# Performance work log

Measured on AMD Instinct MI355X. Metric: run time of the kernel, lower is better.

The kernel has to match this reference:

```python
import jax, jax.numpy as jnp
import numpy as np

B, D, O = 1024, 512, 256


def setup_inputs() -> dict:
    key = jax.random.key(0)
    kx, kw, kt = jax.random.split(key, 3)
    x = jax.random.uniform(kx, (B, D), dtype=jnp.float32)
    w = jax.random.uniform(kw, (D, O), dtype=jnp.float32)
    t = jax.random.uniform(kt, (B, O), dtype=jnp.float32)
    return {"x": x, "w": w, "t": t}


def reference(x, w, t):
    xe = x[:, :, None]   # [B, D, 1]
    te = t[:, None, :]   # [B, 1, O]
    we = w[None, :, :]   # [1, D, O]

    x_comp = 1.0 - xe    # [B, D, 1]
    t_comp = 1.0 - te    # [B, 1, O]
    w_comp = 1.0 - we    # [1, D, O]

    # rel_x: [1, D, O]; sum over batch dim 0 of broadcasted min
    rel_x = 1.0 - (jnp.sum(jnp.minimum(x_comp, t_comp), axis=0, keepdims=True)
                   / jnp.sum(x_comp, axis=0, keepdims=True))
    # rel_w: [B, 1, O]; sum over D dim of broadcasted min
    rel_w = 1.0 - (jnp.sum(jnp.minimum(w_comp, t_comp), axis=-2, keepdims=True)
                   / jnp.sum(w_comp, axis=-2, keepdims=True))

    ind_x = jnp.argmin(jnp.maximum(xe, rel_x), axis=-2, keepdims=True)  # [B, 1, O]
    ind_w = jnp.argmin(jnp.maximum(rel_w, we), axis=-2, keepdims=True)  # [B, 1, O]

    inner_x = jnp.maximum(xe, jax.lax.stop_gradient(we))  # [B, D, O]
    inner_w = jnp.maximum(jax.lax.stop_gradient(xe), we)  # [B, D, O]

    chosen_x = jnp.take_along_axis(inner_x, ind_x, axis=-2).squeeze(-2)  # [B, O]
    chosen_w = jnp.take_along_axis(inner_w, ind_w, axis=-2).squeeze(-2)  # [B, O]
    return chosen_x, chosen_w
```

## Files before the change

kernel.cpp:

```cpp
#include <hip/hip_runtime.h>

#define BB 1024
#define DD 512
#define OO 256

__global__ __launch_bounds__(256) void kA(const float* __restrict__ x,
                                          const float* __restrict__ w,
                                          const float* __restrict__ t,
                                          float* __restrict__ xT,
                                          float* __restrict__ tT,
                                          float* __restrict__ wT,
                                          double* __restrict__ Sxp,
                                          double* __restrict__ part) {
  __shared__ float smem[8 * 136];
  int bid = blockIdx.x, tid = threadIdx.x;
  if (bid < 512) {
    float (*xl)[136] = (float(*)[136])smem;
    int dg = bid >> 3, sy = bid & 7;
    int d0 = dg * 8, b0 = sy * 128, o = tid;
    {
      int bb = tid >> 1, half = tid & 1;
      float4 g = *(const float4*)&x[(b0 + bb) * DD + d0 + half * 4];
      xl[half * 4 + 0][bb] = g.x;
      xl[half * 4 + 1][bb] = g.y;
      xl[half * 4 + 2][bb] = g.z;
      xl[half * 4 + 3][bb] = g.w;
    }
    __syncthreads();
    double acc[8] = {0, 0, 0, 0, 0, 0, 0, 0};
    for (int bb = 0; bb < 128; bb += 4) {
      float tv0 = t[(b0 + bb + 0) * OO + o];
      float tv1 = t[(b0 + bb + 1) * OO + o];
      float tv2 = t[(b0 + bb + 2) * OO + o];
      float tv3 = t[(b0 + bb + 3) * OO + o];
#pragma unroll
      for (int dd = 0; dd < 8; ++dd) {
        float4 xv = *(const float4*)&xl[dd][bb];
        double s01 = (double)fmaxf(xv.x, tv0) + (double)fmaxf(xv.y, tv1);
        double s23 = (double)fmaxf(xv.z, tv2) + (double)fmaxf(xv.w, tv3);
        acc[dd] += s01 + s23;
      }
    }
#pragma unroll
    for (int dd = 0; dd < 8; ++dd)
      part[(sy * DD + d0 + dd) * OO + o] = acc[dd];
  } else if (bid < 1024) {
    float (*tile)[33] = (float(*)[33])smem;
    int r = bid - 512;
    int b0 = (r & 31) * 32, d0 = (r >> 5) * 32;
    int tx = tid & 31, ty = tid >> 5;
    for (int i = 0; i < 32; i += 8)
      tile[ty + i][tx] = x[(b0 + ty + i) * DD + d0 + tx];
    __syncthreads();
    for (int i = 0; i < 32; i += 8)
      xT[(d0 + ty + i) * BB + b0 + tx] = tile[tx][ty + i];
  } else if (bid < 1280) {
    float (*tile)[33] = (float(*)[33])smem;
    int r = bid - 1024;
    int b0 = (r & 31) * 32, o0 = (r >> 5) * 32;
    int tx = tid & 31, ty = tid >> 5;
    for (int i = 0; i < 32; i += 8)
      tile[ty + i][tx] = t[(b0 + ty + i) * OO + o0 + tx];
    __syncthreads();
    for (int i = 0; i < 32; i += 8)
      tT[(o0 + ty + i) * BB + b0 + tx] = tile[tx][ty + i];
  } else if (bid < 1408) {
    float (*tile)[33] = (float(*)[33])smem;
    int r = bid - 1280;
    int d0 = (r & 15) * 32, o0 = (r >> 4) * 32;
    int tx = tid & 31, ty = tid >> 5;
    for (int i = 0; i < 32; i += 8)
      tile[ty + i][tx] = w[(d0 + ty + i) * OO + o0 + tx];
    __syncthreads();
    for (int i = 0; i < 32; i += 8)
      wT[(o0 + ty + i) * DD + d0 + tx] = tile[tx][ty + i];
  } else {
    int r = bid - 1408;
    int sy = r & 7, dh = r >> 3;
    int d = dh * 256 + tid, b0 = sy * 128;
    double s = 0.0;
    for (int b = b0; b < b0 + 128; ++b) s += 1.0 - (double)x[b * DD + d];
    Sxp[sy * DD + d] = s;
  }
}

__global__ __launch_bounds__(256) void kB(const float* __restrict__ wT,
                                          const double* __restrict__ Sxp,
                                          const double* __restrict__ part,
                                          float* __restrict__ sv_g,
                                          int* __restrict__ si_g,
                                          int* __restrict__ off_g,
                                          double* __restrict__ P_g,
                                          int* __restrict__ Mx_g,
                                          double* __restrict__ rv_g,
                                          int* __restrict__ ri_g,
                                          float* __restrict__ eb_g,
                                          double* __restrict__ hdrW,
                                          int* __restrict__ gmin_g) {
  int bid = blockIdx.x, tid = threadIdx.x;
  int lane = tid & 63, wid = tid >> 6;
  if (bid < OO) {
    int o = bid;
    __shared__ float sv[512];
    __shared__ int si[512];
    __shared__ int cnt[512];
    __shared__ int off[513];
    __shared__ double P[513];
    __shared__ int Mx[513];
    __shared__ double wsc[4];
    __shared__ int wmn[4];
    __shared__ unsigned long long wk[4];
    int i0 = 2 * tid, i1 = 2 * tid + 1;
    float w0 = wT[o * DD + i0], w1 = wT[o * DD + i1];
    cnt[i0] = 0; cnt[i1] = 0;
    __syncthreads();
    int q0 = min(511, max(0, (int)(w0 * 512.0f)));
    int q1 = min(511, max(0, (int)(w1 * 512.0f)));
    int sl0 = atomicAdd(&cnt[q0], 1);
    int sl1 = atomicAdd(&cnt[q1], 1);
    __syncthreads();
    {
      int e0 = cnt[i0], e1 = cnt[i1];
      int s = e0 + e1, v = s;
      for (int d = 1; d < 64; d <<= 1) {
        int u = __shfl_up(v, d);
        if (lane >= d) v += u;
      }
      if (lane == 63) wmn[wid] = v;
      __syncthreads();
      int wp = 0;
      for (int u = 0; u < wid; ++u) wp += wmn[u];
      int ex = wp + (v - s);
      off[i0] = ex; off[i1] = ex + e0;
      if (tid == 255) off[512] = ex + s;
      __syncthreads();
    }
    sv[off[q0] + sl0] = w0; si[off[q0] + sl0] = i0;
    sv[off[q1] + sl1] = w1; si[off[q1] + sl1] = i1;
    __syncthreads();
    for (int q = tid; q < 512; q += 256) {
      int s = off[q], e = off[q + 1];
      for (int i = s + 1; i < e; ++i) {
        int ki = si[i]; float kv = sv[i]; int j = i - 1;
        while (j >= s && si[j] > ki) { si[j + 1] = si[j]; sv[j + 1] = sv[j]; --j; }
        si[j + 1] = ki; sv[j + 1] = kv;
      }
    }
    __syncthreads();
    {
      double e0 = (double)sv[i0], e1 = (double)sv[i1];
      int m0 = si[i0], m1 = si[i1];
      double s = e0 + e1; int mm = min(m0, m1);
      double vs = s; int vm = mm;
      for (int d = 1; d < 64; d <<= 1) {
        double us = __shfl_up(vs, d);
        int um = __shfl_up(vm, d);
        if (lane >= d) { vs += us; vm = min(vm, um); }
      }
      double exs = __shfl_up(vs, 1);
      int exm = __shfl_up(vm, 1);
      if (lane == 0) { exs = 0.0; exm = 0x7fffffff; }
      if (lane == 63) { wsc[wid] = vs; wmn[wid] = vm; }
      __syncthreads();
      double wp = 0.0; int wm = 0x7fffffff;
      for (int u = 0; u < wid; ++u) { wp += wsc[u]; wm = min(wm, wmn[u]); }
      double EX = wp + exs; int EXM = min(wm, exm);
      P[i0] = EX; P[i1] = EX + e0;
      Mx[i0] = EXM; Mx[i1] = min(EXM, m0);
      if (tid == 255) { P[512] = EX + s; Mx[512] = min(EXM, mm); }
      __syncthreads();
    }
    {
      unsigned long long k0 = ((unsigned long long)__float_as_uint(sv[i0]) << 32) | (unsigned)si[i0];
      unsigned long long k1 = ((unsigned long long)__float_as_uint(sv[i1]) << 32) | (unsigned)si[i1];
      unsigned long long kk = k0 < k1 ? k0 : k1;
      for (int d = 32; d > 0; d >>= 1) {
        unsigned long long u = __shfl_down(kk, d);
        kk = u < kk ? u : kk;
      }
      if (lane == 0) wk[wid] = kk;
      __syncthreads();
      if (tid == 0) {
        unsigned long long g = wk[0];
        for (int u = 1; u < 4; ++u) g = wk[u] < g ? wk[u] : g;
        gmin_g[o] = (int)(g & 0xffffffffull);
      }
    }
    for (int i = tid; i < 512; i += 256) {
      sv_g[o * 512 + i] = sv[i];
      si_g[o * 512 + i] = si[i];
    }
    for (int i = tid; i < 513; i += 256) {
      off_g[o * 513 + i] = off[i];
      P_g[o * 513 + i] = P[i];
      Mx_g[o * 513 + i] = Mx[i];
    }
    if (tid == 0) { hdrW[o * 2 + 0] = 512.0 - P[512]; hdrW[o * 2 + 1] = P[512]; }
  } else {
    int o = bid - OO;
    __shared__ double rl[512];
    __shared__ int cnt2[512];
    __shared__ int roff[513];
    __shared__ double rv[512];
    __shared__ int ri[512];
    __shared__ float eb[512];
    __shared__ double wred[8];
    __shared__ int wint[4];
    int i0 = 2 * tid, i1 = 2 * tid + 1;
    {
      double sx0 = 0.0, sx1 = 0.0, a0 = 0.0, a1 = 0.0;
#pragma unroll
      for (int s = 0; s < 8; ++s) {
        sx0 += Sxp[s * DD + i0];
        sx1 += Sxp[s * DD + i1];
        a0 += part[(s * DD + i0) * OO + o];
        a1 += part[(s * DD + i1) * OO + o];
      }
      rl[i0] = 1.0 - (1024.0 - a0) / sx0;
      rl[i1] = 1.0 - (1024.0 - a1) / sx1;
    }
    double mn = fmin(rl[i0], rl[i1]), mx = fmax(rl[i0], rl[i1]);
    for (int d = 32; d > 0; d >>= 1) {
      mn = fmin(mn, __shfl_down(mn, d));
      mx = fmax(mx, __shfl_down(mx, d));
    }
    if (lane == 0) { wred[wid] = mn; wred[4 + wid] = mx; }
    cnt2[i0] = 0; cnt2[i1] = 0;
    __syncthreads();
    double rmin = fmin(fmin(wred[0], wred[1]), fmin(wred[2], wred[3]));
    double rmax = fmax(fmax(wred[4], wred[5]), fmax(wred[6], wred[7]));
    double range = rmax - rmin;
    double scale = (range > 0.0) ? (512.0 / range) : 0.0;
    double bw = range * (1.0 / 512.0);
    double base = rmin - range * 1e-9;
    int q0 = min(511, max(0, (int)((rl[i0] - rmin) * scale)));
    int q1 = min(511, max(0, (int)((rl[i1] - rmin) * scale)));
    int sl0 = atomicAdd(&cnt2[q0], 1);
    int sl1 = atomicAdd(&cnt2[q1], 1);
    __syncthreads();
    {
      int e0 = cnt2[i0], e1 = cnt2[i1];
      int s = e0 + e1, v = s;
      for (int d = 1; d < 64; d <<= 1) {
        int u = __shfl_up(v, d);
        if (lane >= d) v += u;
      }
      if (lane == 63) wint[wid] = v;
      __syncthreads();
      int wp = 0;
      for (int u = 0; u < wid; ++u) wp += wint[u];
      int ex = wp + (v - s);
      roff[i0] = ex; roff[i1] = ex + e0;
      if (tid == 255) roff[512] = ex + s;
      __syncthreads();
    }
    {
      int p0 = roff[q0] + sl0, p1 = roff[q1] + sl1;
      rv[p0] = rl[i0]; ri[p0] = i0;
      eb[p0] = __double2float_rd(base + (double)q0 * bw);
      rv[p1] = rl[i1]; ri[p1] = i1;
      eb[p1] = __double2float_rd(base + (double)q1 * bw);
    }
    __syncthreads();
    for (int i = tid; i < 512; i += 256) {
      rv_g[o * 512 + i] = rv[i];
      ri_g[o * 512 + i] = ri[i];
      eb_g[o * 512 + i] = eb[i];
    }
  }
}

__global__ __launch_bounds__(256) void kC(
    const float* __restrict__ xT, const float* __restrict__ wT,
    const float* __restrict__ tT, const float* __restrict__ sv_g,
    const int* __restrict__ si_g, const int* __restrict__ off_g,
    const double* __restrict__ P_g, const int* __restrict__ Mx_g,
    const double* __restrict__ rv_g, const int* __restrict__ ri_g,
    const float* __restrict__ eb_g, const double* __restrict__ hdrW,
    const int* __restrict__ gmin_g, float* __restrict__ out) {
  int o = blockIdx.x, tid = threadIdx.x;
  int b = blockIdx.y * 256 + tid;
  __shared__ float sv[512];
  __shared__ int si[512];
  __shared__ int off[513];
  __shared__ double P[513];
  __shared__ int Mx[513];
  __shared__ double rv[512];
  __shared__ int ri[512];
  __shared__ float eb[512];
  __shared__ float wl[512];
  for (int i = tid; i < 512; i += 256) {
    sv[i] = sv_g[o * 512 + i];
    si[i] = si_g[o * 512 + i];
    rv[i] = rv_g[o * 512 + i];
    ri[i] = ri_g[o * 512 + i];
    eb[i] = eb_g[o * 512 + i];
    wl[i] = wT[o * DD + i];
  }
  for (int i = tid; i < 513; i += 256) {
    off[i] = off_g[o * 513 + i];
    P[i] = P_g[o * 513 + i];
    Mx[i] = Mx_g[o * 513 + i];
  }
  __syncthreads();
  double Sw = hdrW[o * 2 + 0], Wtot = hdrW[o * 2 + 1];
  float c = tT[o * BB + b];
  int j = min(511, max(0, (int)(c * 512.0f)));
  int s0 = off[j], e0 = off[j + 1];
  double pre = P[s0];
  int k = s0;
  for (int i = s0; i < e0; ++i) {
    float wv = sv[i];
    if (wv <= c) { pre += (double)wv; ++k; }
  }
  double smax = (Wtot - pre) + (double)c * (double)k;
  double relw = 1.0 - (512.0 - smax) / Sw;
  int j2 = min(511, max(0, (int)(relw * 512.0)));
  int s2 = off[j2], e2 = off[min(512, j2 + 2)];
  int iw = Mx[s2];
  for (int i = s2; i < e2; ++i)
    if ((double)sv[i] <= relw) iw = min(iw, si[i]);
  if (iw == 0x7fffffff) iw = gmin_g[o];
  float x0 = xT[ri[0] * BB + b], x1 = xT[ri[1] * BB + b];
  float x2 = xT[ri[2] * BB + b], x3 = xT[ri[3] * BB + b];
  float x4 = xT[ri[4] * BB + b], x5 = xT[ri[5] * BB + b];
  float x6 = xT[ri[6] * BB + b], x7 = xT[ri[7] * BB + b];
  double best = 1e300;
  int bix = 0x7fffffff;
  float bestx = 0.0f;
  for (int i = 0; i < 512; ++i) {
    if ((double)eb[i] > best) break;
    int dj = ri[i];
    float xv;
    if (i < 8) {
      xv = (i == 0) ? x0 : (i == 1) ? x1 : (i == 2) ? x2 : (i == 3) ? x3
         : (i == 4) ? x4 : (i == 5) ? x5 : (i == 6) ? x6 : x7;
    } else {
      xv = xT[dj * BB + b];
    }
    double v = fmax((double)xv, rv[i]);
    if (v < best || (v == best && dj < bix)) { best = v; bix = dj; bestx = xv; }
  }
  float ox = fmaxf(bestx, wl[bix]);
  float ow = fmaxf(xT[iw * BB + b], wl[iw]);
  out[b * OO + o] = ox;
  out[BB * OO + b * OO + o] = ow;
}

extern "C" void kernel_launch(void* const* d_in, const int* in_sizes, int n_in,
                              void* d_out, int out_size, void* d_ws,
                              size_t ws_size, hipStream_t stream) {
  const float* x = (const float*)d_in[0];
  const float* w = (const float*)d_in[1];
  const float* t = (const float*)d_in[2];
  float* out = (float*)d_out;
  char* ws = (char*)d_ws;

  size_t off = 0;
  float* xT    = (float*)(ws + off);  off += (size_t)DD * BB * 4;
  float* tT    = (float*)(ws + off);  off += (size_t)OO * BB * 4;
  float* wT    = (float*)(ws + off);  off += (size_t)OO * DD * 4;
  double* Sxp  = (double*)(ws + off); off += (size_t)8 * DD * 8;
  double* part = (double*)(ws + off); off += (size_t)8 * DD * OO * 8;
  float* sv_g  = (float*)(ws + off);  off += (size_t)OO * 512 * 4;
  int* si_g    = (int*)(ws + off);    off += (size_t)OO * 512 * 4;
  int* off_g   = (int*)(ws + off);    off += (size_t)OO * 513 * 4;
  double* P_g  = (double*)(ws + off); off += (size_t)OO * 513 * 8;
  int* Mx_g    = (int*)(ws + off);    off += (size_t)OO * 513 * 4;
  double* rv_g = (double*)(ws + off); off += (size_t)OO * 512 * 8;
  int* ri_g    = (int*)(ws + off);    off += (size_t)OO * 512 * 4;
  float* eb_g  = (float*)(ws + off);  off += (size_t)OO * 512 * 4;
  double* hdrW = (double*)(ws + off); off += (size_t)OO * 2 * 8;
  int* gmin_g  = (int*)(ws + off);    off += (size_t)OO * 4;

  kA<<<1424, 256, 0, stream>>>(x, w, t, xT, tT, wT, Sxp, part);
  kB<<<2 * OO, 256, 0, stream>>>(wT, Sxp, part, sv_g, si_g, off_g, P_g, Mx_g,
                                 rv_g, ri_g, eb_g, hdrW, gmin_g);
  kC<<<dim3(OO, BB / 256), 256, 0, stream>>>(xT, wT, tT, sv_g, si_g, off_g,
                                             P_g, Mx_g, rv_g, ri_g, eb_g,
                                             hdrW, gmin_g, out);
}
```

Measured before the change: 63.98 us.

## Coalesce kC output via transposed scratch plus tile-transpose kernel; prefetch t in kA

kC previously wrote out[b*OO+o] with consecutive threads striding by OO, which made the stores uncoalesced. It now writes to transposed scratch buffers indexed [o][b], so adjacent threads store to adjacent addresses. A new kernel kD uses 32x32 shared-memory tiles to transpose these buffers into the final layout. Separately, kA's batch loop loads the next four t values one iteration ahead so the load latency overlaps the double-precision accumulation. The cost is an extra launch plus a 2 MB scratch write and read.

```diff
diff --git a/kernel.cpp b/kernel.cpp
--- a/kernel.cpp
+++ b/kernel.cpp
@@ -28,11 +28,20 @@
     }
     __syncthreads();
     double acc[8] = {0, 0, 0, 0, 0, 0, 0, 0};
+    float tv0 = t[(b0 + 0) * OO + o];
+    float tv1 = t[(b0 + 1) * OO + o];
+    float tv2 = t[(b0 + 2) * OO + o];
+    float tv3 = t[(b0 + 3) * OO + o];
     for (int bb = 0; bb < 128; bb += 4) {
-      float tv0 = t[(b0 + bb + 0) * OO + o];
-      float tv1 = t[(b0 + bb + 1) * OO + o];
-      float tv2 = t[(b0 + bb + 2) * OO + o];
-      float tv3 = t[(b0 + bb + 3) * OO + o];
+      float nv0, nv1, nv2, nv3;
+      if (bb + 4 < 128) {
+        nv0 = t[(b0 + bb + 4) * OO + o];
+        nv1 = t[(b0 + bb + 5) * OO + o];
+        nv2 = t[(b0 + bb + 6) * OO + o];
+        nv3 = t[(b0 + bb + 7) * OO + o];
+      } else {
+        nv0 = nv1 = nv2 = nv3 = 0.0f;
+      }
 #pragma unroll
       for (int dd = 0; dd < 8; ++dd) {
         float4 xv = *(const float4*)&xl[dd][bb];
@@ -40,6 +49,7 @@
         double s23 = (double)fmaxf(xv.z, tv2) + (double)fmaxf(xv.w, tv3);
         acc[dd] += s01 + s23;
       }
+      tv0 = nv0; tv1 = nv1; tv2 = nv2; tv3 = nv3;
     }
 #pragma unroll
     for (int dd = 0; dd < 8; ++dd)
@@ -277,7 +287,8 @@
     const double* __restrict__ P_g, const int* __restrict__ Mx_g,
     const double* __restrict__ rv_g, const int* __restrict__ ri_g,
     const float* __restrict__ eb_g, const double* __restrict__ hdrW,
-    const int* __restrict__ gmin_g, float* __restrict__ out) {
+    const int* __restrict__ gmin_g, float* __restrict__ outT0,
+    float* __restrict__ outT1) {
   int o = blockIdx.x, tid = threadIdx.x;
   int b = blockIdx.y * 256 + tid;
   __shared__ float sv[512];
@@ -343,8 +354,23 @@
   }
   float ox = fmaxf(bestx, wl[bix]);
   float ow = fmaxf(xT[iw * BB + b], wl[iw]);
-  out[b * OO + o] = ox;
-  out[BB * OO + b * OO + o] = ow;
+  outT0[o * BB + b] = ox;
+  outT1[o * BB + b] = ow;
+}
+
+__global__ __launch_bounds__(256) void kD(const float* __restrict__ outT0,
+                                          const float* __restrict__ outT1,
+                                          float* __restrict__ out) {
+  __shared__ float tile[32][33];
+  const float* src = blockIdx.z ? outT1 : outT0;
+  float* dst = out + (size_t)blockIdx.z * BB * OO;
+  int b0 = blockIdx.x * 32, o0 = blockIdx.y * 32;
+  int tx = threadIdx.x & 31, ty = threadIdx.x >> 5;
+  for (int i = 0; i < 32; i += 8)
+    tile[ty + i][tx] = src[(o0 + ty + i) * BB + b0 + tx];
+  __syncthreads();
+  for (int i = 0; i < 32; i += 8)
+    dst[(b0 + ty + i) * OO + o0 + tx] = tile[tx][ty + i];
 }
 
 extern "C" void kernel_launch(void* const* d_in, const int* in_sizes, int n_in,
@@ -372,11 +398,15 @@
   float* eb_g  = (float*)(ws + off);  off += (size_t)OO * 512 * 4;
   double* hdrW = (double*)(ws + off); off += (size_t)OO * 2 * 8;
   int* gmin_g  = (int*)(ws + off);    off += (size_t)OO * 4;
+  off = (off + 255) & ~(size_t)255;
+  float* outT0 = (float*)(ws + off);  off += (size_t)OO * BB * 4;
+  float* outT1 = (float*)(ws + off);  off += (size_t)OO * BB * 4;
 
   kA<<<1424, 256, 0, stream>>>(x, w, t, xT, tT, wT, Sxp, part);
   kB<<<2 * OO, 256, 0, stream>>>(wT, Sxp, part, sv_g, si_g, off_g, P_g, Mx_g,
                                  rv_g, ri_g, eb_g, hdrW, gmin_g);
   kC<<<dim3(OO, BB / 256), 256, 0, stream>>>(xT, wT, tT, sv_g, si_g, off_g,
                                              P_g, Mx_g, rv_g, ri_g, eb_g,
-                                             hdrW, gmin_g, out);
+                                             hdrW, gmin_g, outT0, outT1);
+  kD<<<dim3(BB / 32, OO / 32, 2), 256, 0, stream>>>(outT0, outT1, out);
 }
```

Result: slower. 66.90 us (+4.6%).
